# Kernel optimization log

Hardware: AMD Instinct MI355X
Metric: run time of the kernel (lower is better)

The kernel has to match this reference:

```python
import jax, jax.numpy as jnp
import numpy as np

H = 1024          # hidden_size
E = 2 * H         # expansion e
S_DIM = 128       # shared q/k dim s
B, S = 4, 2048


def setup_inputs() -> dict:
    key = jax.random.key(0)
    ks = jax.random.split(key, 6)
    inputs = jax.random.normal(ks[0], (B, S, H), dtype=jnp.float32)
    W_uv = jax.random.normal(ks[1], (H, 2 * E + S_DIM), dtype=jnp.float32) * (1.0 / np.sqrt(H))
    b_uv = jnp.zeros((2 * E + S_DIM,), dtype=jnp.float32)
    gamma = jax.random.normal(ks[2], (2, S_DIM), dtype=jnp.float32) * 0.02
    beta = jnp.zeros((2, S_DIM), dtype=jnp.float32)
    W_out = jax.random.normal(ks[3], (E, H), dtype=jnp.float32) * (1.0 / np.sqrt(E))
    b_out = jnp.zeros((H,), dtype=jnp.float32)
    return {"inputs": inputs, "W_uv": W_uv, "b_uv": b_uv,
            "gamma": gamma, "beta": beta, "W_out": W_out, "b_out": b_out}


def reference(inputs, W_uv, b_uv, gamma, beta, W_out, b_out):
    seq_len = inputs.shape[1]
    # uv projection + SiLU
    uvb = jax.nn.silu(jnp.einsum('bsh,hf->bsf', inputs, W_uv) + b_uv)
    u = uvb[..., :E]                       # [B,S,E]
    v = uvb[..., E:2 * E]                  # [B,S,E]
    base = uvb[..., 2 * E:]                # [B,S,s]
    # per-head affine: [B,S,1,s]*[2,s] + [2,s] -> [B,S,2,s]
    qk = base[..., None, :] * gamma + beta
    q, k = qk[..., 0, :], qk[..., 1, :]    # [B,S,s] each
    scores = jnp.einsum('bns,bms->bnm', q, k) / seq_len   # [B,S,S]
    sq = jnp.square(jax.nn.relu(scores))
    attn_v = jnp.einsum('bnm,bme->bne', sq, v)            # [B,S,E]
    return jnp.einsum('bne,eh->bnh', u * attn_v, W_out) + b_out
```

## Files before the change

kernel.cpp:

```cpp
#include <hip/hip_runtime.h>
#include <stdint.h>


#define H_DIM  1024
#define E_DIM  2048
#define SD     128
#define B_SZ   4
#define S_LEN  2048
#define M_TOT  (B_SZ * S_LEN)
#define F_DIM  (2 * E_DIM + SD)

typedef _Float16 f16;
typedef __attribute__((ext_vector_type(4))) _Float16 f16x4;
typedef __attribute__((ext_vector_type(8))) _Float16 f16x8;
typedef __attribute__((ext_vector_type(16))) float f32x16;

__device__ __forceinline__ float silu_f(float x) { return x / (1.f + __expf(-x)); }

__device__ __forceinline__ void gload16(const void* g, void* l) {
  __builtin_amdgcn_global_load_lds(
      (const __attribute__((address_space(1))) void*)(uintptr_t)g,
      (__attribute__((address_space(3))) void*)(uint32_t)(uintptr_t)l,
      16, 0, 0);
}

__global__ __launch_bounds__(256) void cast_f16_k(const float* __restrict__ src,
                                                  f16* __restrict__ dst, long n) {
  long i = ((long)blockIdx.x * 256 + threadIdx.x) * 4;
  if (i < n) {
    float4 v = *(const float4*)(src + i);
    f16x4 h; h[0] = (f16)v.x; h[1] = (f16)v.y; h[2] = (f16)v.z; h[3] = (f16)v.w;
    *(f16x4*)(dst + i) = h;
  }
}

__global__ __launch_bounds__(256) void transpose_cast_k(const float* __restrict__ src,
                                                        f16* __restrict__ dst, int R, int C) {
  __shared__ float tile[32][33];
  int c0 = blockIdx.x * 32, r0 = blockIdx.y * 32;
  int tx = threadIdx.x & 31, ty = threadIdx.x >> 5;
  for (int i = ty; i < 32; i += 8) tile[i][tx] = src[(long)(r0 + i) * C + c0 + tx];
  __syncthreads();
  for (int i = ty; i < 32; i += 8) dst[(long)(c0 + i) * R + r0 + tx] = (f16)tile[tx][i];
}

template <int MODE>
__global__ __launch_bounds__(256) void mfma_gemm(
    const f16* __restrict__ Ag, const f16* __restrict__ Bg,
    float* __restrict__ F0, f16* __restrict__ H0, const f16* __restrict__ H1,
    f16* __restrict__ H2, f16* __restrict__ H3,
    const float* __restrict__ C0, const float* __restrict__ C1,
    const float* __restrict__ C2)
{
  constexpr int K   = (MODE == 1) ? SD : (MODE == 0 || MODE == 4) ? H_DIM : 2048;
  constexpr int LDA = K, LDB = K;

  __shared__ f16 As[2][128][32];
  __shared__ f16 Bs[2][128][32];

  const int t    = threadIdx.x;
  const int w    = t >> 6;
  const int lane = t & 63;
  const int lo5  = lane & 31;
  const int hi   = lane >> 5;
  const int wy   = w >> 1, wx = w & 1;
  const int m0   = blockIdx.y * 128;
  const int n0   = blockIdx.x * 128;
  const long z   = blockIdx.z;

  const f16* A = Ag + (MODE == 1 ? z * (long)S_LEN * SD
                     : MODE == 2 ? z * (long)S_LEN * S_LEN : 0);
  const f16* B = Bg + (MODE == 1 ? z * (long)S_LEN * SD
                     : MODE == 2 ? z * (long)E_DIM * S_LEN : 0);

  const int srow = lane >> 2;
  const int scol = (((lane & 3) ^ ((srow >> 1) & 3))) * 8;
  const int rsw  = (lo5 >> 1) & 3;

  f32x16 acc[2][2] = {};

  for (int k0 = 0; k0 < K; k0 += 64) {
#pragma unroll
    for (int h = 0; h < 2; h++)
#pragma unroll
      for (int g16 = 0; g16 < 2; g16++) {
        const int r = (w << 5) + (g16 << 4);
        gload16(A + (long)(m0 + r + srow) * LDA + k0 + (h << 5) + scol, &As[h][r][0]);
        gload16(B + (long)(n0 + r + srow) * LDB + k0 + (h << 5) + scol, &Bs[h][r][0]);
      }
    __syncthreads();

#pragma unroll
    for (int ks = 0; ks < 4; ks++) {
      const int h  = ks >> 1;
      const int cl = ((ks & 1) << 1) + hi;
      const int kc = (cl ^ rsw) << 3;
      f16x8 av[2], bv[2];
#pragma unroll
      for (int i = 0; i < 2; i++)
        av[i] = *(const f16x8*)&As[h][(wy << 6) + (i << 5) + lo5][kc];
#pragma unroll
      for (int j = 0; j < 2; j++)
        bv[j] = *(const f16x8*)&Bs[h][(wx << 6) + (j << 5) + lo5][kc];
#pragma unroll
      for (int i = 0; i < 2; i++)
#pragma unroll
        for (int j = 0; j < 2; j++)
          acc[i][j] = __builtin_amdgcn_mfma_f32_32x32x16_f16(av[i], bv[j], acc[i][j], 0, 0, 0);
    }
    __syncthreads();
  }

  const int rb0 = m0 + (wy << 6) + (hi << 2);
  const int cb0 = n0 + (wx << 6) + lo5;

  if (MODE == 0) {
    if (n0 < E_DIM) {
#pragma unroll
      for (int i = 0; i < 2; i++)
#pragma unroll
        for (int j = 0; j < 2; j++) {
          int gc = cb0 + (j << 5);
          float bias = C0[gc];
#pragma unroll
          for (int g = 0; g < 4; g++)
#pragma unroll
            for (int rr = 0; rr < 4; rr++) {
              int gr = rb0 + (i << 5) + (g << 3) + rr;
              H0[(long)gr * E_DIM + gc] = (f16)silu_f(acc[i][j][g * 4 + rr] + bias);
            }
        }
    } else {
#pragma unroll
      for (int i = 0; i < 2; i++) {
#pragma unroll
        for (int j = 0; j < 2; j++) {
          int gc = cb0 + (j << 5);
          float bias = C0[gc];
#pragma unroll
          for (int g = 0; g < 4; g++) {
            int gr0 = rb0 + (i << 5) + (g << 3);
            int b   = gr0 >> 11;
            int s0  = gr0 & (S_LEN - 1);
            f16x4 pk;
#pragma unroll
            for (int rr = 0; rr < 4; rr++) pk[rr] = (f16)silu_f(acc[i][j][g * 4 + rr] + bias);
            *(f16x4*)&H1[((long)b * E_DIM + (gc - E_DIM)) * S_LEN + s0] = pk;
          }
        }
      }
    }
  } else if (MODE == 4) {
#pragma unroll
    for (int i = 0; i < 2; i++)
#pragma unroll
      for (int j = 0; j < 2; j++) {
        int jj = cb0 + (j << 5);
        float bias = C0[jj];
        float g0 = C1[jj], g1 = C1[SD + jj];
        float be0 = C2[jj], be1 = C2[SD + jj];
#pragma unroll
        for (int g = 0; g < 4; g++)
#pragma unroll
          for (int rr = 0; rr < 4; rr++) {
            int gr = rb0 + (i << 5) + (g << 3) + rr;
            float s = silu_f(acc[i][j][g * 4 + rr] + bias);
            H2[(long)gr * SD + jj] = (f16)(s * g0 + be0);
            H3[(long)gr * SD + jj] = (f16)(s * g1 + be1);
          }
      }
  } else if (MODE == 1) {
#pragma unroll
    for (int i = 0; i < 2; i++)
#pragma unroll
      for (int j = 0; j < 2; j++) {
        int gc = cb0 + (j << 5);
#pragma unroll
        for (int g = 0; g < 4; g++)
#pragma unroll
          for (int rr = 0; rr < 4; rr++) {
            int gr = rb0 + (i << 5) + (g << 3) + rr;
            float tv = fmaxf(acc[i][j][g * 4 + rr], 0.f) * 64.f;
            H0[z * (long)S_LEN * S_LEN + (long)gr * S_LEN + gc] = (f16)(tv * tv);
          }
      }
  } else if (MODE == 2) {
    const long rowoff = z * S_LEN;
#pragma unroll
    for (int i = 0; i < 2; i++)
#pragma unroll
      for (int j = 0; j < 2; j++) {
        int gc = cb0 + (j << 5);
#pragma unroll
        for (int g = 0; g < 4; g++)
#pragma unroll
          for (int rr = 0; rr < 4; rr++) {
            int gr = rb0 + (i << 5) + (g << 3) + rr;
            long idx = (rowoff + gr) * (long)E_DIM + gc;
            H0[idx] = (f16)((float)H1[idx] * acc[i][j][g * 4 + rr]);
          }
      }
  } else {
#pragma unroll
    for (int i = 0; i < 2; i++)
#pragma unroll
      for (int j = 0; j < 2; j++) {
        int gc = cb0 + (j << 5);
        float bias = C0[gc];
#pragma unroll
        for (int g = 0; g < 4; g++)
#pragma unroll
          for (int rr = 0; rr < 4; rr++) {
            int gr = rb0 + (i << 5) + (g << 3) + rr;
            F0[(long)gr * H_DIM + gc] = acc[i][j][g * 4 + rr] * (1.0f / 17179869184.0f) + bias;
          }
      }
  }
}

extern "C" void kernel_launch(void* const* d_in, const int* in_sizes, int n_in,
                              void* d_out, int out_size, void* d_ws, size_t ws_size,
                              hipStream_t stream) {
  const float* X     = (const float*)d_in[0];
  const float* W_uv  = (const float*)d_in[1];
  const float* b_uv  = (const float*)d_in[2];
  const float* gamma = (const float*)d_in[3];
  const float* beta  = (const float*)d_in[4];
  const float* W_out = (const float*)d_in[5];
  const float* b_out = (const float*)d_in[6];
  float* out = (float*)d_out;

  char* wp = (char*)d_ws;
  f16* Xh   = (f16*)wp; wp += (long)M_TOT * H_DIM * 2;
  f16* Wuvt = (f16*)wp; wp += (long)F_DIM * H_DIM * 2;
  f16* Wt   = (f16*)wp; wp += (long)H_DIM * E_DIM * 2;
  f16* u    = (f16*)wp; wp += (long)M_TOT * E_DIM * 2;
  f16* vt   = (f16*)wp; wp += (long)M_TOT * E_DIM * 2;
  f16* qh   = (f16*)wp; wp += (long)M_TOT * SD * 2;
  f16* kh   = (f16*)wp; wp += (long)M_TOT * SD * 2;
  f16* sq   = (f16*)wp; wp += (long)B_SZ * S_LEN * S_LEN * 2;
  f16* p    = (f16*)wp; wp += (long)M_TOT * E_DIM * 2;

  cast_f16_k<<<(M_TOT * H_DIM) / (256 * 4), 256, 0, stream>>>(X, Xh, (long)M_TOT * H_DIM);
  transpose_cast_k<<<dim3(F_DIM / 32, H_DIM / 32), 256, 0, stream>>>(W_uv, Wuvt, H_DIM, F_DIM);
  transpose_cast_k<<<dim3(H_DIM / 32, E_DIM / 32), 256, 0, stream>>>(W_out, Wt, E_DIM, H_DIM);

  mfma_gemm<0><<<dim3(2 * E_DIM / 128, M_TOT / 128, 1), 256, 0, stream>>>(
      Xh, Wuvt, nullptr, u, vt, nullptr, nullptr, b_uv, nullptr, nullptr);

  mfma_gemm<4><<<dim3(1, M_TOT / 128, 1), 256, 0, stream>>>(
      Xh, Wuvt + (long)2 * E_DIM * H_DIM, nullptr, nullptr, nullptr, qh, kh,
      b_uv + 2 * E_DIM, gamma, beta);

  mfma_gemm<1><<<dim3(S_LEN / 128, S_LEN / 128, B_SZ), 256, 0, stream>>>(
      qh, kh, nullptr, sq, nullptr, nullptr, nullptr, nullptr, nullptr, nullptr);

  mfma_gemm<2><<<dim3(E_DIM / 128, S_LEN / 128, B_SZ), 256, 0, stream>>>(
      sq, vt, nullptr, p, u, nullptr, nullptr, nullptr, nullptr, nullptr);

  mfma_gemm<3><<<dim3(H_DIM / 128, M_TOT / 128, 1), 256, 0, stream>>>(
      p, Wt, out, nullptr, nullptr, nullptr, nullptr, b_out, nullptr, nullptr);
}
```

Measured before the change: 368.6 us.

## Fuse prep kernels and merge qk projection into uv GEMM launch

Combines the X cast and both weight transpose-casts into one prep kernel, and folds the separate q/k projection GEMM into the main uv GEMM by extending its grid by one column tile, with a third epilogue branch applying SiLU plus gamma/beta. This removes three kernel launches and lets the small qk GEMM (64 blocks) run alongside the large one instead of serially with poor occupancy. It also adds a launch_bounds occupancy hint of 4 blocks per CU, which may constrain registers for all GEMM modes.

```diff
diff --git a/kernel.cpp b/kernel.cpp
--- a/kernel.cpp
+++ b/kernel.cpp
@@ -24,20 +24,30 @@
       16, 0, 0);
 }
 
-__global__ __launch_bounds__(256) void cast_f16_k(const float* __restrict__ src,
-                                                  f16* __restrict__ dst, long n) {
-  long i = ((long)blockIdx.x * 256 + threadIdx.x) * 4;
-  if (i < n) {
-    float4 v = *(const float4*)(src + i);
+__global__ __launch_bounds__(256) void prep_k(
+    const float* __restrict__ X, f16* __restrict__ Xh,
+    const float* __restrict__ Wuv, f16* __restrict__ Wuvt,
+    const float* __restrict__ Wout, f16* __restrict__ Wt)
+{
+  const int b = blockIdx.x;
+  if (b < 8192) {
+    long i = ((long)b * 256 + threadIdx.x) * 4;
+    float4 v = *(const float4*)(X + i);
     f16x4 h; h[0] = (f16)v.x; h[1] = (f16)v.y; h[2] = (f16)v.z; h[3] = (f16)v.w;
-    *(f16x4*)(dst + i) = h;
-  }
-}
-
-__global__ __launch_bounds__(256) void transpose_cast_k(const float* __restrict__ src,
-                                                        f16* __restrict__ dst, int R, int C) {
+    *(f16x4*)(Xh + i) = h;
+    return;
+  }
   __shared__ float tile[32][33];
-  int c0 = blockIdx.x * 32, r0 = blockIdx.y * 32;
+  const float* src; f16* dst; int R, C, c0, r0;
+  if (b < 8192 + 4224) {
+    int idx = b - 8192;
+    src = Wuv; dst = Wuvt; R = H_DIM; C = F_DIM;
+    c0 = (idx % 132) * 32; r0 = (idx / 132) * 32;
+  } else {
+    int idx = b - 8192 - 4224;
+    src = Wout; dst = Wt; R = E_DIM; C = H_DIM;
+    c0 = (idx % 32) * 32; r0 = (idx / 32) * 32;
+  }
   int tx = threadIdx.x & 31, ty = threadIdx.x >> 5;
   for (int i = ty; i < 32; i += 8) tile[i][tx] = src[(long)(r0 + i) * C + c0 + tx];
   __syncthreads();
@@ -45,14 +55,14 @@
 }
 
 template <int MODE>
-__global__ __launch_bounds__(256) void mfma_gemm(
+__global__ __launch_bounds__(256, 4) void mfma_gemm(
     const f16* __restrict__ Ag, const f16* __restrict__ Bg,
     float* __restrict__ F0, f16* __restrict__ H0, const f16* __restrict__ H1,
     f16* __restrict__ H2, f16* __restrict__ H3,
     const float* __restrict__ C0, const float* __restrict__ C1,
     const float* __restrict__ C2)
 {
-  constexpr int K   = (MODE == 1) ? SD : (MODE == 0 || MODE == 4) ? H_DIM : 2048;
+  constexpr int K   = (MODE == 1) ? SD : (MODE == 0) ? H_DIM : 2048;
   constexpr int LDA = K, LDB = K;
 
   __shared__ f16 As[2][128][32];
@@ -130,7 +140,7 @@
               H0[(long)gr * E_DIM + gc] = (f16)silu_f(acc[i][j][g * 4 + rr] + bias);
             }
         }
-    } else {
+    } else if (n0 < 2 * E_DIM) {
 #pragma unroll
       for (int i = 0; i < 2; i++) {
 #pragma unroll
@@ -149,26 +159,27 @@
           }
         }
       }
+    } else {
+#pragma unroll
+      for (int i = 0; i < 2; i++)
+#pragma unroll
+        for (int j = 0; j < 2; j++) {
+          int gc = cb0 + (j << 5);
+          int jj = gc - 2 * E_DIM;
+          float bias = C0[gc];
+          float g0 = C1[jj], g1 = C1[SD + jj];
+          float be0 = C2[jj], be1 = C2[SD + jj];
+#pragma unroll
+          for (int g = 0; g < 4; g++)
+#pragma unroll
+            for (int rr = 0; rr < 4; rr++) {
+              int gr = rb0 + (i << 5) + (g << 3) + rr;
+              float s = silu_f(acc[i][j][g * 4 + rr] + bias);
+              H2[(long)gr * SD + jj] = (f16)(s * g0 + be0);
+              H3[(long)gr * SD + jj] = (f16)(s * g1 + be1);
+            }
+        }
     }
-  } else if (MODE == 4) {
-#pragma unroll
-    for (int i = 0; i < 2; i++)
-#pragma unroll
-      for (int j = 0; j < 2; j++) {
-        int jj = cb0 + (j << 5);
-        float bias = C0[jj];
-        float g0 = C1[jj], g1 = C1[SD + jj];
-        float be0 = C2[jj], be1 = C2[SD + jj];
-#pragma unroll
-        for (int g = 0; g < 4; g++)
-#pragma unroll
-          for (int rr = 0; rr < 4; rr++) {
-            int gr = rb0 + (i << 5) + (g << 3) + rr;
-            float s = silu_f(acc[i][j][g * 4 + rr] + bias);
-            H2[(long)gr * SD + jj] = (f16)(s * g0 + be0);
-            H3[(long)gr * SD + jj] = (f16)(s * g1 + be1);
-          }
-      }
   } else if (MODE == 1) {
 #pragma unroll
     for (int i = 0; i < 2; i++)
@@ -241,16 +252,10 @@
   f16* sq   = (f16*)wp; wp += (long)B_SZ * S_LEN * S_LEN * 2;
   f16* p    = (f16*)wp; wp += (long)M_TOT * E_DIM * 2;
 
-  cast_f16_k<<<(M_TOT * H_DIM) / (256 * 4), 256, 0, stream>>>(X, Xh, (long)M_TOT * H_DIM);
-  transpose_cast_k<<<dim3(F_DIM / 32, H_DIM / 32), 256, 0, stream>>>(W_uv, Wuvt, H_DIM, F_DIM);
-  transpose_cast_k<<<dim3(H_DIM / 32, E_DIM / 32), 256, 0, stream>>>(W_out, Wt, E_DIM, H_DIM);
-
-  mfma_gemm<0><<<dim3(2 * E_DIM / 128, M_TOT / 128, 1), 256, 0, stream>>>(
-      Xh, Wuvt, nullptr, u, vt, nullptr, nullptr, b_uv, nullptr, nullptr);
-
-  mfma_gemm<4><<<dim3(1, M_TOT / 128, 1), 256, 0, stream>>>(
-      Xh, Wuvt + (long)2 * E_DIM * H_DIM, nullptr, nullptr, nullptr, qh, kh,
-      b_uv + 2 * E_DIM, gamma, beta);
+  prep_k<<<8192 + 4224 + 2048, 256, 0, stream>>>(X, Xh, W_uv, Wuvt, W_out, Wt);
+
+  mfma_gemm<0><<<dim3(F_DIM / 128, M_TOT / 128, 1), 256, 0, stream>>>(
+      Xh, Wuvt, nullptr, u, vt, qh, kh, b_uv, gamma, beta);
 
   mfma_gemm<1><<<dim3(S_LEN / 128, S_LEN / 128, B_SZ), 256, 0, stream>>>(
       qh, kh, nullptr, sq, nullptr, nullptr, nullptr, nullptr, nullptr, nullptr);
```

Result: slower. 386.5 us (+4.9%).
